# Optimization experiments

Hardware: AMD Instinct MI355X
Metric: run time of the kernel (lower is better)

## Reference

```python
import jax, jax.numpy as jnp
import numpy as np

N, E = 50000, 640000
FEAT, EMB, HID, B = 128, 128, 512, 32


def setup_inputs() -> dict:
    key = jax.random.key(0)
    ks = jax.random.split(key, 12)
    def w(k, shape, fan_in):
        return jax.random.normal(k, shape, dtype=jnp.float32) / np.sqrt(fan_in)
    return {
        "x": jax.random.normal(ks[0], (N, FEAT), dtype=jnp.float32),
        "edge_index": jax.random.randint(ks[1], (2, E), 0, N, dtype=jnp.int64),
        "last_hidden": jax.random.normal(ks[2], (1, B, HID), dtype=jnp.float32),
        "W1_rel": w(ks[3], (FEAT, EMB), FEAT),
        "W1_root": w(ks[4], (FEAT, EMB), FEAT),
        "b1": jnp.zeros((EMB,), dtype=jnp.float32),
        "W2_rel": w(ks[5], (EMB, EMB), EMB),
        "W2_root": w(ks[6], (EMB, EMB), EMB),
        "b2": jnp.zeros((EMB,), dtype=jnp.float32),
        "Wp": w(ks[7], (HID, EMB), HID),
        "bp": jnp.zeros((EMB,), dtype=jnp.float32),
    }


def _rgcn(h, src, dst, W_rel, W_root, b):
    # transform-then-gather (N < E so cheaper): messages along edges src->dst
    msg = (h @ W_rel)[src]                                   # [E, emb]
    agg = jax.ops.segment_sum(msg, dst, num_segments=N)      # [N, emb]
    deg = jax.ops.segment_sum(jnp.ones((E,), h.dtype), dst, num_segments=N)
    agg = agg / jnp.maximum(deg, 1.0)[:, None]               # mean aggregation (PyG RGCNConv default)
    return agg + h @ W_root + b


def reference(x, edge_index, last_hidden, W1_rel, W1_root, b1, W2_rel, W2_root, b2, Wp, bp):
    src, dst = edge_index[0], edge_index[1]
    h = jax.nn.relu(_rgcn(x, src, dst, W1_rel, W1_root, b1))   # [N, emb]
    h = jax.nn.relu(_rgcn(h, src, dst, W2_rel, W2_root, b2))   # [N, emb]
    message_embed = (last_hidden @ Wp + bp)[0]                 # squeeze(0) -> [B, emb]
    scores = h @ message_embed.T                               # [N, B]
    return jax.nn.log_softmax(scores, axis=0)
```

## Files before the change

### kernel.cpp

```cpp
#include <hip/hip_runtime.h>
#include <hip/hip_bf16.h>

#define N_NODES 50000
#define N_EDGES 640000
#define DUMMY   N_NODES
#define PAD_SSRC 990000

typedef __attribute__((ext_vector_type(8))) short short8;
typedef __attribute__((ext_vector_type(4))) float floatx4;

__device__ __forceinline__ float bf2f(unsigned short u) {
    return __uint_as_float(((unsigned int)u) << 16);
}
__device__ __forceinline__ unsigned short f2bf(float x) {
    unsigned int u = __float_as_uint(x);
    u = (u + 0x7fffu + ((u >> 16) & 1u)) >> 16;
    return (unsigned short)u;
}
__device__ __forceinline__ unsigned char f2f8(float x) {
    int pk = __builtin_amdgcn_cvt_pk_fp8_f32(x, x, 0, false);
    return (unsigned char)(pk & 0xff);
}
__device__ __forceinline__ unsigned int pk4_fp8(float x0, float x1, float x2, float x3) {
    int v = __builtin_amdgcn_cvt_pk_fp8_f32(x0, x1, 0, false);
    v = __builtin_amdgcn_cvt_pk_fp8_f32(x2, x3, v, true);
    return (unsigned int)v;
}
__device__ __forceinline__ unsigned int pk2_bf16(float lo, float hi) {
    return (unsigned int)f2bf(lo) | ((unsigned int)f2bf(hi) << 16);
}

__global__ void __launch_bounds__(256) prep_k(const float* __restrict__ W0,
                                              const float* __restrict__ W1,
                                              const float* __restrict__ W2,
                                              const float* __restrict__ W3,
                                              unsigned short* __restrict__ T0,
                                              unsigned short* __restrict__ T1,
                                              unsigned short* __restrict__ T2,
                                              unsigned short* __restrict__ T3,
                                              int* __restrict__ cnt,
                                              const float* __restrict__ lh,
                                              const float* __restrict__ Wp,
                                              const float* __restrict__ bp,
                                              unsigned short* __restrict__ meb,
                                              unsigned short* __restrict__ ssrc,
                                              unsigned char* __restrict__ tbf,
                                              int* __restrict__ total,
                                              const int* __restrict__ dst,
                                              int* __restrict__ rank) {
    int b = blockIdx.x, tid = threadIdx.x;
    bool is_hist;
    int idx;
    if (b < 4414) { is_hist = ((b & 1) == 0); idx = b >> 1; }
    else          { is_hist = true;            idx = 2207 + (b - 4414); }
    if (is_hist) {
        int e = idx * 256 + tid;
        int d = dst[e];
        int r = atomicAdd(&cnt[d], 1);
        rank[e] = (r << 16) | d;
        return;
    }
    int s = idx;
    if (s < 256) {
        int i2 = s * 256 + tid;
        int w = i2 >> 14;
        int r = i2 & 16383;
        int n = r >> 7, k = r & 127;
        const float* W = (w == 0) ? W0 : (w == 1) ? W1 : (w == 2) ? W2 : W3;
        unsigned short* T = (w == 0) ? T0 : (w == 1) ? T1 : (w == 2) ? T2 : T3;
        T[r] = f2bf(W[k * 128 + n]);
    } else if (s < 272) {
        int o = (s - 256) * 256 + tid;
        int i = o >> 7, c = o & 127;
        float acc = bp[c];
        const float4* lr = (const float4*)(lh + i * 512);
        #pragma unroll 4
        for (int k4 = 0; k4 < 128; k4++) {
            float4 v = lr[k4];
            acc += v.x * Wp[(4 * k4 + 0) * 128 + c] + v.y * Wp[(4 * k4 + 1) * 128 + c]
                 + v.z * Wp[(4 * k4 + 2) * 128 + c] + v.w * Wp[(4 * k4 + 3) * 128 + c];
        }
        meb[o] = f2bf(acc);
    } else if (s < 2206) {
        int i = (s - 272) * 256 + tid;
        if (i < PAD_SSRC / 2) ((unsigned int*)ssrc)[i] = 0xC350C350u;
    } else {
        if (tid < 32) ((unsigned int*)(tbf + (size_t)DUMMY * 128))[tid] = 0;
        else if (tid == 32) *total = 0;
    }
}

#define EPI_LD 132
template <bool AF32>
__device__ __forceinline__ void gemm_dual_lds32(int bid, int tid,
                                                const void* __restrict__ Ain,
                                                const unsigned short* __restrict__ BtRel,
                                                const unsigned short* __restrict__ BtRoot,
                                                unsigned char* __restrict__ Trel,
                                                unsigned short* __restrict__ Rootb,
                                                int M, char* __restrict__ pool) {
    int wid = tid >> 6, lane = tid & 63;
    int m = lane & 15, g = lane >> 4;
    int r0 = bid * 32;
    if constexpr (AF32) {
        const float* A = (const float*)Ain;
        #pragma unroll
        for (int j = 0; j < 2; j++) {
            int k = j * 256 + tid;
            int row = k >> 4;
            int grow = r0 + row; grow = (grow < M) ? grow : (M - 1);
            const float* p = A + (size_t)grow * 128 + (k & 15) * 8;
            float4 v0 = *(const float4*)p;
            float4 v1 = *(const float4*)(p + 4);
            short8 t8;
            t8[0] = (short)f2bf(v0.x); t8[1] = (short)f2bf(v0.y);
            t8[2] = (short)f2bf(v0.z); t8[3] = (short)f2bf(v0.w);
            t8[4] = (short)f2bf(v1.x); t8[5] = (short)f2bf(v1.y);
            t8[6] = (short)f2bf(v1.z); t8[7] = (short)f2bf(v1.w);
            *(short8*)(pool + ((k * 16) ^ ((row & 7) << 4))) = t8;
        }
    } else {
        const unsigned short* A = (const unsigned short*)Ain;
        #pragma unroll
        for (int j = 0; j < 2; j++) {
            int k = j * 256 + tid;
            int row = k >> 4;
            int grow = r0 + row; grow = (grow < M) ? grow : (M - 1);
            short8 v = *(const short8*)(A + (size_t)grow * 128 + (k & 15) * 8);
            *(short8*)(pool + ((k * 16) ^ ((row & 7) << 4))) = v;
        }
    }
    #pragma unroll
    for (int j = 0; j < 8; j++) {
        int k = j * 256 + tid;
        int row = k >> 4;
        short8 v = *(const short8*)(BtRel + (size_t)k * 8);
        *(short8*)(pool + 8192 + ((k * 16) ^ ((row & 7) << 4))) = v;
    }
    __syncthreads();
    int lrow = (wid >> 1) * 16 + m;
    int asw = (lrow & 7) << 4, abase = lrow * 256;
    short8 a[4];
    #pragma unroll
    for (int kt = 0; kt < 4; kt++)
        a[kt] = *(const short8*)(pool + ((abase + kt * 64 + g * 16) ^ asw));
    int browbase = (wid & 1) * 64;
    floatx4 accR[4], accO[4];
    #pragma unroll
    for (int ct = 0; ct < 4; ct++) {
        accR[ct] = (floatx4)(0.f);
        int brow = browbase + ct * 16 + m;
        int bbase = brow * 256, bsw = (brow & 7) << 4;
        #pragma unroll
        for (int kt = 0; kt < 4; kt++) {
            short8 bv = *(const short8*)(pool + 8192 + ((bbase + kt * 64 + g * 16) ^ bsw));
            accR[ct] = __builtin_amdgcn_mfma_f32_16x16x32_bf16(a[kt], bv, accR[ct], 0, 0, 0);
        }
    }
    __syncthreads();
    #pragma unroll
    for (int j = 0; j < 8; j++) {
        int k = j * 256 + tid;
        int row = k >> 4;
        short8 v = *(const short8*)(BtRoot + (size_t)k * 8);
        *(short8*)(pool + 8192 + ((k * 16) ^ ((row & 7) << 4))) = v;
    }
    __syncthreads();
    #pragma unroll
    for (int ct = 0; ct < 4; ct++) {
        accO[ct] = (floatx4)(0.f);
        int brow = browbase + ct * 16 + m;
        int bbase = brow * 256, bsw = (brow & 7) << 4;
        #pragma unroll
        for (int kt = 0; kt < 4; kt++) {
            short8 bv = *(const short8*)(pool + 8192 + ((bbase + kt * 64 + g * 16) ^ bsw));
            accO[ct] = __builtin_amdgcn_mfma_f32_16x16x32_bf16(a[kt], bv, accO[ct], 0, 0, 0);
        }
    }
    __syncthreads();
    float* epi = (float*)(pool + 8192);
    int rh = (wid >> 1) * 16, ch = (wid & 1) * 64;
    #pragma unroll
    for (int ct = 0; ct < 4; ct++)
        #pragma unroll
        for (int rg = 0; rg < 4; rg++)
            epi[(rh + g * 4 + rg) * EPI_LD + ch + ct * 16 + m] = accR[ct][rg];
    __syncthreads();
    {
        int lr = tid >> 3, c0 = (tid & 7) * 16;
        int ro = r0 + lr;
        const float* row = epi + lr * EPI_LD + c0;
        if (ro < M) {
            uint4 w;
            w.x = pk4_fp8(row[0],  row[1],  row[2],  row[3]);
            w.y = pk4_fp8(row[4],  row[5],  row[6],  row[7]);
            w.z = pk4_fp8(row[8],  row[9],  row[10], row[11]);
            w.w = pk4_fp8(row[12], row[13], row[14], row[15]);
            *(uint4*)(Trel + (size_t)ro * 128 + c0) = w;
        }
    }
    __syncthreads();
    #pragma unroll
    for (int ct = 0; ct < 4; ct++)
        #pragma unroll
        for (int rg = 0; rg < 4; rg++)
            epi[(rh + g * 4 + rg) * EPI_LD + ch + ct * 16 + m] = accO[ct][rg];
    __syncthreads();
    {
        int lr = tid >> 3, c0 = (tid & 7) * 16;
        int ro = r0 + lr;
        const float* row = epi + lr * EPI_LD + c0;
        if (ro < M) {
            uint4 w0, w1;
            w0.x = pk2_bf16(row[0],  row[1]);
            w0.y = pk2_bf16(row[2],  row[3]);
            w0.z = pk2_bf16(row[4],  row[5]);
            w0.w = pk2_bf16(row[6],  row[7]);
            w1.x = pk2_bf16(row[8],  row[9]);
            w1.y = pk2_bf16(row[10], row[11]);
            w1.z = pk2_bf16(row[12], row[13]);
            w1.w = pk2_bf16(row[14], row[15]);
            *(uint4*)(Rootb + (size_t)ro * 128 + c0) = w0;
            *(uint4*)(Rootb + (size_t)ro * 128 + c0 + 8) = w1;
        }
    }
}

__global__ void __launch_bounds__(256) allocgemm_k(const int* __restrict__ cnt,
                                                   int* __restrict__ prow,
                                                   int* __restrict__ total,
                                                   const float* __restrict__ A,
                                                   const unsigned short* __restrict__ BtRel,
                                                   const unsigned short* __restrict__ BtRoot,
                                                   unsigned char* __restrict__ Trel,
                                                   unsigned short* __restrict__ Rootb) {
    __shared__ __align__(16) char pool[40960];
    if (blockIdx.x < 196) {
        int* sm = (int*)pool;
        int* base_s = (int*)(pool + 1024);
        int t = threadIdx.x;
        int i = blockIdx.x * 256 + t;
        int pc = (i < N_NODES) ? ((cnt[i] + 7) & ~7) : 0;
        sm[t] = pc;
        __syncthreads();
        for (int off = 1; off < 256; off <<= 1) {
            int v = (t >= off) ? sm[t - off] : 0;
            __syncthreads();
            sm[t] += v;
            __syncthreads();
        }
        if (t == 255) *base_s = atomicAdd(total, sm[255]);
        __syncthreads();
        if (i < N_NODES) prow[i] = *base_s + sm[t] - pc;
    } else {
        gemm_dual_lds32<true>(blockIdx.x - 196, threadIdx.x, A, BtRel, BtRoot,
                              Trel, Rootb, N_NODES, pool);
    }
}

__global__ void __launch_bounds__(256) place_k(const int* __restrict__ src,
                                               const int* __restrict__ prow,
                                               const int* __restrict__ rank,
                                               unsigned short* __restrict__ ssrc) {
    int e = blockIdx.x * 256 + threadIdx.x;
    if (e < N_EDGES) {
        int pk = rank[e];
        int d = pk & 0xffff;
        int r = pk >> 16;
        ssrc[prow[d] + r] = (unsigned short)src[e];
    }
}

__global__ void __launch_bounds__(256) gemm_dual_k(const unsigned short* __restrict__ A,
                                                   const unsigned short* __restrict__ BtRel,
                                                   const unsigned short* __restrict__ BtRoot,
                                                   unsigned char* __restrict__ Trel,
                                                   unsigned short* __restrict__ Rootb, int M) {
    __shared__ __align__(16) char pool[40960];
    gemm_dual_lds32<false>(blockIdx.x, threadIdx.x, A, BtRel, BtRoot, Trel, Rootb, M, pool);
}

__global__ void __launch_bounds__(256) agg_k(const int* __restrict__ prow,
                                             const int* __restrict__ cnt,
                                             const unsigned short* __restrict__ ssrc,
                                             const unsigned char* __restrict__ t,
                                             const unsigned short* __restrict__ rootb,
                                             const float* __restrict__ bias,
                                             unsigned short* __restrict__ hout) {
    int node = blockIdx.x * 4 + (threadIdx.x >> 6);
    if (node >= N_NODES) return;
    int lane = threadIdx.x & 63;
    int fl = lane & 31;
    int sh = (lane & 32) >> 1;
    int beg = prow[node];
    int deg = cnt[node];
    int endp = beg + ((deg + 7) & ~7);
    const unsigned char* tf = t + fl * 4;
    float a0=0.f,a1=0.f,a2=0.f,a3=0.f;
    float b0=0.f,b1=0.f,b2=0.f,b3=0.f;
    for (int e = beg; e < endp; e += 16) {
        uint4 w0 = *(const uint4*)(ssrc + e);
        uint4 w1 = (e + 8 < endp) ? *(const uint4*)(ssrc + e + 8)
                                  : make_uint4(0xC350C350u, 0xC350C350u, 0xC350C350u, 0xC350C350u);
        int i0 = (int)((w0.x >> sh) & 0xffffu);
        int i1 = (int)((w0.y >> sh) & 0xffffu);
        int i2 = (int)((w0.z >> sh) & 0xffffu);
        int i3 = (int)((w0.w >> sh) & 0xffffu);
        int i4 = (int)((w1.x >> sh) & 0xffffu);
        int i5 = (int)((w1.y >> sh) & 0xffffu);
        int i6 = (int)((w1.z >> sh) & 0xffffu);
        int i7 = (int)((w1.w >> sh) & 0xffffu);
        unsigned int u0 = *(const unsigned int*)(tf + (size_t)i0 * 128);
        unsigned int u1 = *(const unsigned int*)(tf + (size_t)i1 * 128);
        unsigned int u2 = *(const unsigned int*)(tf + (size_t)i2 * 128);
        unsigned int u3 = *(const unsigned int*)(tf + (size_t)i3 * 128);
        unsigned int u4 = *(const unsigned int*)(tf + (size_t)i4 * 128);
        unsigned int u5 = *(const unsigned int*)(tf + (size_t)i5 * 128);
        unsigned int u6 = *(const unsigned int*)(tf + (size_t)i6 * 128);
        unsigned int u7 = *(const unsigned int*)(tf + (size_t)i7 * 128);
        a0 += __builtin_amdgcn_cvt_f32_fp8(u0, 0) + __builtin_amdgcn_cvt_f32_fp8(u1, 0);
        a1 += __builtin_amdgcn_cvt_f32_fp8(u0, 1) + __builtin_amdgcn_cvt_f32_fp8(u1, 1);
        a2 += __builtin_amdgcn_cvt_f32_fp8(u0, 2) + __builtin_amdgcn_cvt_f32_fp8(u1, 2);
        a3 += __builtin_amdgcn_cvt_f32_fp8(u0, 3) + __builtin_amdgcn_cvt_f32_fp8(u1, 3);
        b0 += __builtin_amdgcn_cvt_f32_fp8(u2, 0) + __builtin_amdgcn_cvt_f32_fp8(u3, 0);
        b1 += __builtin_amdgcn_cvt_f32_fp8(u2, 1) + __builtin_amdgcn_cvt_f32_fp8(u3, 1);
        b2 += __builtin_amdgcn_cvt_f32_fp8(u2, 2) + __builtin_amdgcn_cvt_f32_fp8(u3, 2);
        b3 += __builtin_amdgcn_cvt_f32_fp8(u2, 3) + __builtin_amdgcn_cvt_f32_fp8(u3, 3);
        a0 += __builtin_amdgcn_cvt_f32_fp8(u4, 0) + __builtin_amdgcn_cvt_f32_fp8(u5, 0);
        a1 += __builtin_amdgcn_cvt_f32_fp8(u4, 1) + __builtin_amdgcn_cvt_f32_fp8(u5, 1);
        a2 += __builtin_amdgcn_cvt_f32_fp8(u4, 2) + __builtin_amdgcn_cvt_f32_fp8(u5, 2);
        a3 += __builtin_amdgcn_cvt_f32_fp8(u4, 3) + __builtin_amdgcn_cvt_f32_fp8(u5, 3);
        b0 += __builtin_amdgcn_cvt_f32_fp8(u6, 0) + __builtin_amdgcn_cvt_f32_fp8(u7, 0);
        b1 += __builtin_amdgcn_cvt_f32_fp8(u6, 1) + __builtin_amdgcn_cvt_f32_fp8(u7, 1);
        b2 += __builtin_amdgcn_cvt_f32_fp8(u6, 2) + __builtin_amdgcn_cvt_f32_fp8(u7, 2);
        b3 += __builtin_amdgcn_cvt_f32_fp8(u6, 3) + __builtin_amdgcn_cvt_f32_fp8(u7, 3);
    }
    a0 += b0; a1 += b1; a2 += b2; a3 += b3;
    a0 += __shfl_xor(a0, 32);
    a1 += __shfl_xor(a1, 32);
    a2 += __shfl_xor(a2, 32);
    a3 += __shfl_xor(a3, 32);
    if ((lane & 32) == 0) {
        float inv = 1.f / fmaxf((float)deg, 1.f);
        int f = fl * 4;
        ushort4 r = *(const ushort4*)(rootb + (size_t)node * 128 + f);
        float4 bb = *(const float4*)(bias + f);
        ushort4 o;
        o.x = f2bf(fmaxf(a0 * inv + bf2f(r.x) + bb.x, 0.f));
        o.y = f2bf(fmaxf(a1 * inv + bf2f(r.y) + bb.y, 0.f));
        o.z = f2bf(fmaxf(a2 * inv + bf2f(r.z) + bb.z, 0.f));
        o.w = f2bf(fmaxf(a3 * inv + bf2f(r.w) + bb.w, 0.f));
        *(ushort4*)(hout + (size_t)node * 128 + f) = o;
    }
}

__global__ void __launch_bounds__(256) scores_cs_k(const unsigned short* __restrict__ A,
                                                   const unsigned short* __restrict__ Bt,
                                                   float* __restrict__ S,
                                                   float* __restrict__ pm,
                                                   float* __restrict__ ps) {
    __shared__ float Sl[64][33];
    __shared__ float sm[256], ss[256];
    int tid = threadIdx.x;
    int wid = tid >> 6, lane = tid & 63;
    int r0 = blockIdx.x * 64 + wid * 16;
    int m = lane & 15, g = lane >> 4;
    int row = r0 + m;
    int rowc = (row < N_NODES) ? row : (N_NODES - 1);
    short8 a[4];
    #pragma unroll
    for (int kt = 0; kt < 4; kt++)
        a[kt] = *(const short8*)(A + (size_t)rowc * 128 + kt * 32 + g * 8);
    floatx4 acc[2];
    acc[0] = (floatx4)(0.f);
    acc[1] = (floatx4)(0.f);
    #pragma unroll
    for (int ct = 0; ct < 2; ct++) {
        const unsigned short* b = Bt + (size_t)(ct * 16 + m) * 128 + g * 8;
        #pragma unroll
        for (int kt = 0; kt < 4; kt++) {
            short8 bv = *(const short8*)(b + kt * 32);
            acc[ct] = __builtin_amdgcn_mfma_f32_16x16x32_bf16(a[kt], bv, acc[ct], 0, 0, 0);
        }
    }
    #pragma unroll
    for (int ct = 0; ct < 2; ct++) {
        #pragma unroll
        for (int rg = 0; rg < 4; rg++) {
            int lr = wid * 16 + g * 4 + rg;
            int ro = r0 + g * 4 + rg;
            Sl[lr][ct * 16 + m] = acc[ct][rg];
            if (ro < N_NODES) S[(size_t)ro * 32 + ct * 16 + m] = acc[ct][rg];
        }
    }
    __syncthreads();
    int col = tid & 31, sub = tid >> 5;
    int blkbase = blockIdx.x * 64;
    float mm = -3.4e38f, s = 0.f;
    for (int r = sub; r < 64; r += 8) {
        if (blkbase + r < N_NODES) {
            float v = Sl[r][col];
            if (v > mm) { s = s * __expf(mm - v) + 1.f; mm = v; }
            else        { s += __expf(v - mm); }
        }
    }
    sm[tid] = mm; ss[tid] = s;
    __syncthreads();
    for (int off = 128; off >= 32; off >>= 1) {
        if (tid < off) {
            float m2 = sm[tid + off], s2 = ss[tid + off];
            float M = fmaxf(sm[tid], m2);
            ss[tid] = ss[tid] * __expf(sm[tid] - M) + s2 * __expf(m2 - M);
            sm[tid] = M;
        }
        __syncthreads();
    }
    if (tid < 32) { pm[tid * 782 + blockIdx.x] = sm[tid]; ps[tid * 782 + blockIdx.x] = ss[tid]; }
}

__global__ void __launch_bounds__(256) merge_k(const float* __restrict__ pm,
                                               const float* __restrict__ ps,
                                               float* __restrict__ cmg,
                                               float* __restrict__ clg) {
    __shared__ float sm[256], ss[256];
    int col = blockIdx.x;
    int t = threadIdx.x;
    float m = -3.4e38f, s = 0.f;
    for (int c = t; c < 782; c += 256) {
        float m2 = pm[col * 782 + c], s2 = ps[col * 782 + c];
        float M = fmaxf(m, m2);
        s = s * __expf(m - M) + s2 * __expf(m2 - M);
        m = M;
    }
    sm[t] = m; ss[t] = s;
    __syncthreads();
    for (int off = 128; off > 0; off >>= 1) {
        if (t < off) {
            float m2 = sm[t + off], s2 = ss[t + off];
            float M = fmaxf(sm[t], m2);
            ss[t] = ss[t] * __expf(sm[t] - M) + s2 * __expf(m2 - M);
            sm[t] = M;
        }
        __syncthreads();
    }
    if (t == 0) { cmg[col] = sm[0]; clg[col] = logf(ss[0]); }
}

__global__ void __launch_bounds__(256) final_k(const float* __restrict__ S,
                                               const float* __restrict__ cmg,
                                               const float* __restrict__ clg,
                                               float* __restrict__ out) {
    __shared__ float cc[32];
    int t = threadIdx.x;
    if (t < 32) cc[t] = cmg[t] + clg[t];
    __syncthreads();
    int idx = blockIdx.x * 256 + t;
    if (idx < N_NODES * 32) {
        int b = idx & 31;
        out[idx] = S[idx] - cc[b];
    }
}

extern "C" void kernel_launch(void* const* d_in, const int* in_sizes, int n_in,
                              void* d_out, int out_size, void* d_ws, size_t ws_size,
                              hipStream_t stream) {
    const float* x       = (const float*)d_in[0];
    const int*   ei      = (const int*)d_in[1];
    const float* lh      = (const float*)d_in[2];
    const float* W1_rel  = (const float*)d_in[3];
    const float* W1_root = (const float*)d_in[4];
    const float* b1      = (const float*)d_in[5];
    const float* W2_rel  = (const float*)d_in[6];
    const float* W2_root = (const float*)d_in[7];
    const float* b2      = (const float*)d_in[8];
    const float* Wp      = (const float*)d_in[9];
    const float* bp      = (const float*)d_in[10];
    float* out = (float*)d_out;
    float* ws  = (float*)d_ws;

    unsigned char*  tbf   = (unsigned char*)(ws + 3200000);
    unsigned short* rootb = (unsigned short*)(ws + 4800032);
    unsigned short* hb    = (unsigned short*)(ws + 8000032);
    unsigned short* Wt1r  = (unsigned short*)(ws + 11200032);
    unsigned short* Wt1o  = (unsigned short*)(ws + 11208224);
    unsigned short* Wt2r  = (unsigned short*)(ws + 11216416);
    unsigned short* Wt2o  = (unsigned short*)(ws + 11224608);
    unsigned short* MEb   = (unsigned short*)(ws + 11232800);
    float* pm   = ws + 11234848;
    float* ps   = ws + 11259872;
    float* cmg  = ws + 11284896;
    float* clg  = ws + 11284928;
    int*   cnt  = (int*)(ws + 11284960);
    int*   prow = (int*)(ws + 11334960);
    int*   total= (int*)(ws + 11384961);
    int*   rank = (int*)(ws + 11384964);
    unsigned short* ssrc = (unsigned short*)(ws + 12024964);
    float* S    = ws + 12519964;

    const int* srcp = ei;
    const int* dstp = ei + N_EDGES;

    const int e_grid   = (N_EDGES + 255) / 256;
    const int ew_grid  = (N_NODES * 32 + 255) / 256;
    const int agg_grid = (N_NODES + 3) / 4;
    const int mm_grid  = (N_NODES + 63) / 64;
    const int g32_grid = (N_NODES + 31) / 32;

    hipMemsetAsync(cnt, 0, N_NODES * sizeof(int), stream);

    prep_k<<<4707, 256, 0, stream>>>(W1_rel, W1_root, W2_rel, W2_root,
                                     Wt1r, Wt1o, Wt2r, Wt2o,
                                     cnt, lh, Wp, bp, MEb, ssrc, tbf, total,
                                     dstp, rank);

    allocgemm_k<<<196 + g32_grid, 256, 0, stream>>>(cnt, prow, total,
                                                    x, Wt1r, Wt1o, tbf, rootb);

    place_k<<<e_grid, 256, 0, stream>>>(srcp, prow, rank, ssrc);

    agg_k<<<agg_grid, 256, 0, stream>>>(prow, cnt, ssrc, tbf, rootb, b1, hb);

    gemm_dual_k<<<g32_grid, 256, 0, stream>>>(hb, Wt2r, Wt2o, tbf, rootb, N_NODES);

    agg_k<<<agg_grid, 256, 0, stream>>>(prow, cnt, ssrc, tbf, rootb, b2, hb);

    scores_cs_k<<<mm_grid, 256, 0, stream>>>(hb, MEb, S, pm, ps);

    merge_k<<<32, 256, 0, stream>>>(pm, ps, cmg, clg);

    final_k<<<ew_grid, 256, 0, stream>>>(S, cmg, clg, out);
}
```

Measured before the change: 216.8 us.

## Reschedule prep kernels to overlap histogram with layer-1 GEMM; stage score operands in LDS

Splits the old prep kernel into a small weight-prep kernel and a new kernel that interleaves the edge degree histogram and ssrc padding fill with the layer-1 dual GEMM blocks. The prefix-scan allocation moves into its own small kernel that runs after both. The aim is to hide the atomic histogram and memset traffic behind GEMM work. The scores kernel now stages its A and B tiles through swizzled LDS with coalesced loads instead of strided per-lane global reads. The cost is one extra kernel launch and more LDS in the scores kernel.

```diff
diff --git a/kernel.cpp b/kernel.cpp
--- a/kernel.cpp
+++ b/kernel.cpp
@@ -30,47 +30,31 @@
     return (unsigned int)f2bf(lo) | ((unsigned int)f2bf(hi) << 16);
 }
 
-__global__ void __launch_bounds__(256) prep_k(const float* __restrict__ W0,
-                                              const float* __restrict__ W1,
-                                              const float* __restrict__ W2,
-                                              const float* __restrict__ W3,
-                                              unsigned short* __restrict__ T0,
-                                              unsigned short* __restrict__ T1,
-                                              unsigned short* __restrict__ T2,
-                                              unsigned short* __restrict__ T3,
-                                              int* __restrict__ cnt,
-                                              const float* __restrict__ lh,
-                                              const float* __restrict__ Wp,
-                                              const float* __restrict__ bp,
-                                              unsigned short* __restrict__ meb,
-                                              unsigned short* __restrict__ ssrc,
-                                              unsigned char* __restrict__ tbf,
-                                              int* __restrict__ total,
-                                              const int* __restrict__ dst,
-                                              int* __restrict__ rank) {
+__global__ void __launch_bounds__(256) prep0_k(const float* __restrict__ W0,
+                                               const float* __restrict__ W1,
+                                               const float* __restrict__ W2,
+                                               const float* __restrict__ W3,
+                                               unsigned short* __restrict__ T0,
+                                               unsigned short* __restrict__ T1,
+                                               unsigned short* __restrict__ T2,
+                                               unsigned short* __restrict__ T3,
+                                               const float* __restrict__ lh,
+                                               const float* __restrict__ Wp,
+                                               const float* __restrict__ bp,
+                                               unsigned short* __restrict__ meb,
+                                               unsigned char* __restrict__ tbf,
+                                               int* __restrict__ total) {
     int b = blockIdx.x, tid = threadIdx.x;
-    bool is_hist;
-    int idx;
-    if (b < 4414) { is_hist = ((b & 1) == 0); idx = b >> 1; }
-    else          { is_hist = true;            idx = 2207 + (b - 4414); }
-    if (is_hist) {
-        int e = idx * 256 + tid;
-        int d = dst[e];
-        int r = atomicAdd(&cnt[d], 1);
-        rank[e] = (r << 16) | d;
-        return;
-    }
-    int s = idx;
-    if (s < 256) {
-        int i2 = s * 256 + tid;
+    if (b < 256) {
+        int i2 = b * 256 + tid;
         int w = i2 >> 14;
         int r = i2 & 16383;
         int n = r >> 7, k = r & 127;
         const float* W = (w == 0) ? W0 : (w == 1) ? W1 : (w == 2) ? W2 : W3;
         unsigned short* T = (w == 0) ? T0 : (w == 1) ? T1 : (w == 2) ? T2 : T3;
         T[r] = f2bf(W[k * 128 + n]);
-    } else if (s < 272) {
-        int o = (s - 256) * 256 + tid;
+    } else if (b < 272) {
+        int o = (b - 256) * 256 + tid;
         int i = o >> 7, c = o & 127;
         float acc = bp[c];
         const float4* lr = (const float4*)(lh + i * 512);
@@ -81,9 +65,6 @@
                  + v.z * Wp[(4 * k4 + 2) * 128 + c] + v.w * Wp[(4 * k4 + 3) * 128 + c];
         }
         meb[o] = f2bf(acc);
-    } else if (s < 2206) {
-        int i = (s - 272) * 256 + tid;
-        if (i < PAD_SSRC / 2) ((unsigned int*)ssrc)[i] = 0xC350C350u;
     } else {
         if (tid < 32) ((unsigned int*)(tbf + (size_t)DUMMY * 128))[tid] = 0;
         else if (tid == 32) *total = 0;
@@ -226,36 +207,52 @@
     }
 }
 
-__global__ void __launch_bounds__(256) allocgemm_k(const int* __restrict__ cnt,
-                                                   int* __restrict__ prow,
-                                                   int* __restrict__ total,
-                                                   const float* __restrict__ A,
-                                                   const unsigned short* __restrict__ BtRel,
-                                                   const unsigned short* __restrict__ BtRoot,
-                                                   unsigned char* __restrict__ Trel,
-                                                   unsigned short* __restrict__ Rootb) {
+__global__ void __launch_bounds__(256) prep1_k(int* __restrict__ cnt,
+                                               const int* __restrict__ dst,
+                                               int* __restrict__ rank,
+                                               unsigned short* __restrict__ ssrc,
+                                               const float* __restrict__ A,
+                                               const unsigned short* __restrict__ BtRel,
+                                               const unsigned short* __restrict__ BtRoot,
+                                               unsigned char* __restrict__ Trel,
+                                               unsigned short* __restrict__ Rootb) {
     __shared__ __align__(16) char pool[40960];
-    if (blockIdx.x < 196) {
-        int* sm = (int*)pool;
-        int* base_s = (int*)(pool + 1024);
-        int t = threadIdx.x;
-        int i = blockIdx.x * 256 + t;
-        int pc = (i < N_NODES) ? ((cnt[i] + 7) & ~7) : 0;
-        sm[t] = pc;
+    int b = blockIdx.x, tid = threadIdx.x;
+    if ((b & 3) == 3) {
+        gemm_dual_lds32<true>(b >> 2, tid, A, BtRel, BtRoot, Trel, Rootb, N_NODES, pool);
+        return;
+    }
+    int n = (b >> 2) * 3 + (b & 3);
+    if (n < 2500) {
+        int e = n * 256 + tid;
+        int d = dst[e];
+        int r = atomicAdd(&cnt[d], 1);
+        rank[e] = (r << 16) | d;
+    } else if (n < 4434) {
+        int i = (n - 2500) * 256 + tid;
+        if (i < PAD_SSRC / 2) ((unsigned int*)ssrc)[i] = 0xC350C350u;
+    }
+}
+
+__global__ void __launch_bounds__(256) alloc_k(const int* __restrict__ cnt,
+                                               int* __restrict__ prow,
+                                               int* __restrict__ total) {
+    __shared__ int sm[256];
+    __shared__ int base_s;
+    int t = threadIdx.x;
+    int i = blockIdx.x * 256 + t;
+    int pc = (i < N_NODES) ? ((cnt[i] + 7) & ~7) : 0;
+    sm[t] = pc;
+    __syncthreads();
+    for (int off = 1; off < 256; off <<= 1) {
+        int v = (t >= off) ? sm[t - off] : 0;
         __syncthreads();
-        for (int off = 1; off < 256; off <<= 1) {
-            int v = (t >= off) ? sm[t - off] : 0;
-            __syncthreads();
-            sm[t] += v;
-            __syncthreads();
-        }
-        if (t == 255) *base_s = atomicAdd(total, sm[255]);
+        sm[t] += v;
         __syncthreads();
-        if (i < N_NODES) prow[i] = *base_s + sm[t] - pc;
-    } else {
-        gemm_dual_lds32<true>(blockIdx.x - 196, threadIdx.x, A, BtRel, BtRoot,
-                              Trel, Rootb, N_NODES, pool);
-    }
+    }
+    if (t == 255) base_s = atomicAdd(total, sm[255]);
+    __syncthreads();
+    if (i < N_NODES) prow[i] = base_s + sm[t] - pc;
 }
 
 __global__ void __launch_bounds__(256) place_k(const int* __restrict__ src,
@@ -359,27 +356,45 @@
                                                    float* __restrict__ S,
                                                    float* __restrict__ pm,
                                                    float* __restrict__ ps) {
+    __shared__ __align__(16) char stg[24576];
     __shared__ float Sl[64][33];
     __shared__ float sm[256], ss[256];
     int tid = threadIdx.x;
     int wid = tid >> 6, lane = tid & 63;
+    int m = lane & 15, g = lane >> 4;
     int r0 = blockIdx.x * 64 + wid * 16;
-    int m = lane & 15, g = lane >> 4;
-    int row = r0 + m;
-    int rowc = (row < N_NODES) ? row : (N_NODES - 1);
+    #pragma unroll
+    for (int j = 0; j < 4; j++) {
+        int k = j * 256 + tid;
+        int row = k >> 4;
+        int grow = blockIdx.x * 64 + row; grow = (grow < N_NODES) ? grow : (N_NODES - 1);
+        short8 v = *(const short8*)(A + (size_t)grow * 128 + (k & 15) * 8);
+        *(short8*)(stg + ((k * 16) ^ ((row & 7) << 4))) = v;
+    }
+    #pragma unroll
+    for (int j = 0; j < 2; j++) {
+        int k = j * 256 + tid;
+        int row = k >> 4;
+        short8 v = *(const short8*)(Bt + (size_t)k * 8);
+        *(short8*)(stg + 16384 + ((k * 16) ^ ((row & 7) << 4))) = v;
+    }
+    __syncthreads();
+    int lrA = wid * 16 + m;
+    int asw = (lrA & 7) << 4, abase = lrA * 256;
     short8 a[4];
     #pragma unroll
     for (int kt = 0; kt < 4; kt++)
-        a[kt] = *(const short8*)(A + (size_t)rowc * 128 + kt * 32 + g * 8);
+        a[kt] = *(const short8*)(stg + ((abase + kt * 64 + g * 16) ^ asw));
     floatx4 acc[2];
     acc[0] = (floatx4)(0.f);
     acc[1] = (floatx4)(0.f);
     #pragma unroll
     for (int ct = 0; ct < 2; ct++) {
-        const unsigned short* b = Bt + (size_t)(ct * 16 + m) * 128 + g * 8;
+        int brow = ct * 16 + m;
+        int bbase = brow * 256, bsw = (brow & 7) << 4;
         #pragma unroll
         for (int kt = 0; kt < 4; kt++) {
-            short8 bv = *(const short8*)(b + kt * 32);
+            short8 bv = *(const short8*)(stg + 16384 + ((bbase + kt * 64 + g * 16) ^ bsw));
             acc[ct] = __builtin_amdgcn_mfma_f32_16x16x32_bf16(a[kt], bv, acc[ct], 0, 0, 0);
         }
     }
@@ -508,13 +523,14 @@
 
     hipMemsetAsync(cnt, 0, N_NODES * sizeof(int), stream);
 
-    prep_k<<<4707, 256, 0, stream>>>(W1_rel, W1_root, W2_rel, W2_root,
+    prep0_k<<<273, 256, 0, stream>>>(W1_rel, W1_root, W2_rel, W2_root,
                                      Wt1r, Wt1o, Wt2r, Wt2o,
-                                     cnt, lh, Wp, bp, MEb, ssrc, tbf, total,
-                                     dstp, rank);
-
-    allocgemm_k<<<196 + g32_grid, 256, 0, stream>>>(cnt, prow, total,
-                                                    x, Wt1r, Wt1o, tbf, rootb);
+                                     lh, Wp, bp, MEb, tbf, total);
+
+    prep1_k<<<6252, 256, 0, stream>>>(cnt, dstp, rank, ssrc,
+                                      x, Wt1r, Wt1o, tbf, rootb);
+
+    alloc_k<<<196, 256, 0, stream>>>(cnt, prow, total);
 
     place_k<<<e_grid, 256, 0, stream>>>(srcp, prow, rank, ssrc);
 
```

New measurement: 236.3 us. 9.0% more time.
